# Performance work log

Measured on AMD Instinct MI355X. Metric: run time of the kernel, lower is better.

## Reference

```python
import jax, jax.numpy as jnp
import numpy as np

N = 20000          # nodes
E = 320000         # edges (avg degree 16)
G = 256            # graphs in batch
NUM_TACTICS = 1000
NUM_TYPES = 3
TYPE_D = 32
TAC_D = 64
H = 512
IN_D = TYPE_D + TAC_D  # 96


def setup_inputs() -> dict:
    key = jax.random.key(0)
    ks = jax.random.split(key, 16)
    node_type = jax.random.randint(ks[0], (N,), 0, NUM_TYPES)
    # tactic id in {-1, 0..num_tactics-1}
    node_tactic_id = jax.random.randint(ks[1], (N,), 0, NUM_TACTICS + 1) - 1
    edge_index = jax.random.randint(ks[2], (2, E), 0, N)
    batch = jnp.sort(jax.random.randint(ks[3], (N,), 0, G))
    s = 0.02
    p = {
        'type_emb': jax.random.normal(ks[4], (NUM_TYPES, TYPE_D), jnp.float32) * s,
        'tactic_emb': jax.random.normal(ks[5], (NUM_TACTICS + 1, TAC_D), jnp.float32) * s,
        'W1l': jax.random.normal(ks[6], (H, IN_D), jnp.float32) * s,
        'b1l': jnp.zeros((H,), jnp.float32),
        'W1r': jax.random.normal(ks[7], (H, IN_D), jnp.float32) * s,
        'W2l': jax.random.normal(ks[8], (H, H), jnp.float32) * s,
        'b2l': jnp.zeros((H,), jnp.float32),
        'W2r': jax.random.normal(ks[9], (H, H), jnp.float32) * s,
        'Wc1': jax.random.normal(ks[10], (H, H), jnp.float32) * s,
        'bc1': jnp.zeros((H,), jnp.float32),
        'Wc2': jax.random.normal(ks[11], (NUM_TACTICS, H), jnp.float32) * s,
        'bc2': jnp.zeros((NUM_TACTICS,), jnp.float32),
    }
    return dict(node_type=node_type, node_tactic_id=node_tactic_id,
                edge_index=edge_index, batch=batch, **p)


def _sage_conv(x, src, dst, Wl, bl, Wr):
    # PyG SAGEConv (aggr='mean'): out = lin_l(mean_{j in N(i)} x_j) + lin_r(x_i)
    msg = x[src]                                              # [E, D]
    ssum = jax.ops.segment_sum(msg, dst, num_segments=N)      # [N, D]
    cnt = jax.ops.segment_sum(jnp.ones((src.shape[0],), x.dtype), dst,
                              num_segments=N)                 # [N]
    agg = ssum / jnp.maximum(cnt, 1.0)[:, None]
    return agg @ Wl.T + bl + x @ Wr.T


def reference(node_type, node_tactic_id, edge_index, batch,
              type_emb, tactic_emb, W1l, b1l, W1r, W2l, b2l, W2r,
              Wc1, bc1, Wc2, bc2):
    t_type = type_emb[node_type]                              # [N, 32]
    shifted = jnp.clip(node_tactic_id + 1, 0, NUM_TACTICS)
    t_tac = tactic_emb[shifted]                               # [N, 64]
    x = jnp.concatenate([t_type, t_tac], axis=-1)             # [N, 96]

    src, dst = edge_index[0], edge_index[1]
    x = jax.nn.relu(_sage_conv(x, src, dst, W1l, b1l, W1r))   # [N, H]
    x = _sage_conv(x, src, dst, W2l, b2l, W2r)                # [N, H]

    # global mean pool over graphs
    gsum = jax.ops.segment_sum(x, batch, num_segments=G)      # [G, H]
    gcnt = jax.ops.segment_sum(jnp.ones((N,), x.dtype), batch, num_segments=G)
    graph_repr = gsum / jnp.maximum(gcnt, 1.0)[:, None]

    h = jax.nn.relu(graph_repr @ Wc1.T + bc1)
    logits = h @ Wc2.T + bc2                                  # [G, num_tactics]
    return logits
```

## Files before the change

kernel.cpp:

```cpp
#include <hip/hip_runtime.h>

#define N_NODES 20000
#define N_EDGES 320000
#define NGRAPH  256
#define NTAC    1000
#define HD      512
#define NC      25
#define KCH     800

typedef __attribute__((ext_vector_type(8))) short bf16x8;
typedef __attribute__((ext_vector_type(4))) short short4v;
typedef __attribute__((ext_vector_type(4))) float f32x4;

__device__ __forceinline__ short f2bf(float f) {
  union { float f; unsigned u; } v; v.f = f;
  unsigned r = v.u + 0x7FFFu + ((v.u >> 16) & 1u);
  return (short)(r >> 16);
}
__device__ __forceinline__ float bf2f(short s) {
  union { unsigned u; float f; } v;
  v.u = ((unsigned)(unsigned short)s) << 16;
  return v.f;
}
__device__ __forceinline__ bf16x8 cast8(const float* p) {
  float4 v0 = *reinterpret_cast<const float4*>(p);
  float4 v1 = *reinterpret_cast<const float4*>(p + 4);
  bf16x8 o;
  o[0] = f2bf(v0.x); o[1] = f2bf(v0.y); o[2] = f2bf(v0.z); o[3] = f2bf(v0.w);
  o[4] = f2bf(v1.x); o[5] = f2bf(v1.y); o[6] = f2bf(v1.z); o[7] = f2bf(v1.w);
  return o;
}
__device__ __forceinline__ void gload16(const void* g, void* l) {
  __builtin_amdgcn_global_load_lds((const __attribute__((address_space(1))) void*)g,
                                   (__attribute__((address_space(3))) void*)l,
                                   16, 0, 0);
}

__global__ void k_front(const float* __restrict__ Wc1, const float* __restrict__ Wc2,
                        short* __restrict__ WC1B, short* __restrict__ WC2B,
                        const float* __restrict__ W1l, const float* __restrict__ W1r,
                        short* __restrict__ BC1,
                        const float* __restrict__ W2l, const float* __restrict__ W2r,
                        short* __restrict__ BC2,
                        const int* __restrict__ ntype, const int* __restrict__ ntac,
                        const float* __restrict__ temb, const float* __restrict__ tacemb,
                        short* __restrict__ A1,
                        const int* __restrict__ dst, int* __restrict__ deg,
                        const int* __restrict__ batch, int* __restrict__ rstart,
                        float* __restrict__ COEF, short* __restrict__ COEFB) {
  int idx = blockIdx.x * 256 + threadIdx.x;
  const int S0 = HD * HD / 8;
  const int S1 = NTAC * HD / 8;
  const int S2 = HD * 192 / 8;
  const int S3 = HD * 1024 / 8;
  const int S4 = N_NODES * 24;
  const int S5 = N_EDGES;
  const int S6 = N_NODES;
  const int S7 = NGRAPH * N_NODES / 4;
  const int S8 = NGRAPH * N_NODES / 8;
  if (idx < S0) {
    *reinterpret_cast<bf16x8*>(&WC1B[idx * 8]) = cast8(&Wc1[idx * 8]);
  } else if ((idx -= S0) < S1) {
    *reinterpret_cast<bf16x8*>(&WC2B[idx * 8]) = cast8(&Wc2[idx * 8]);
  } else if ((idx -= S1) < S2) {
    int n = idx / 24, k8 = idx - n * 24;
    const float* s = (k8 < 12) ? &W1l[(size_t)n * 96 + k8 * 8]
                               : &W1r[(size_t)n * 96 + (k8 - 12) * 8];
    *reinterpret_cast<bf16x8*>(&BC1[(size_t)n * 192 + k8 * 8]) = cast8(s);
  } else if ((idx -= S2) < S3) {
    int n = idx >> 7, k8 = idx & 127;
    const float* s = (k8 < 64) ? &W2l[(size_t)n * 512 + k8 * 8]
                               : &W2r[(size_t)n * 512 + (k8 - 64) * 8];
    *reinterpret_cast<bf16x8*>(&BC2[(size_t)n * 1024 + k8 * 8]) = cast8(s);
  } else if ((idx -= S3) < S4) {
    int node = idx / 24;
    int j = idx - node * 24;
    float4 v;
    int col;
    if (j < 8) {
      int t = ntype[node];
      v = *reinterpret_cast<const float4*>(&temb[t * 32 + j * 4]);
      col = j * 4;
    } else {
      int s = ntac[node] + 1;
      s = s < 0 ? 0 : (s > NTAC ? NTAC : s);
      v = *reinterpret_cast<const float4*>(&tacemb[s * 64 + (j - 8) * 4]);
      col = 32 + (j - 8) * 4;
    }
    short4v o = {f2bf(v.x), f2bf(v.y), f2bf(v.z), f2bf(v.w)};
    *reinterpret_cast<short4v*>(&A1[(size_t)node * 192 + 96 + col]) = o;
  } else if ((idx -= S4) < S5) {
    atomicAdd(&deg[dst[idx]], 1);
  } else if ((idx -= S5) < S6) {
    int i = idx;
    int b = batch[i];
    int bp = (i == 0) ? -1 : batch[i - 1];
    for (int g = bp + 1; g <= b; ++g) rstart[g] = i;
    if (i == N_NODES - 1)
      for (int g = b + 1; g <= NGRAPH; ++g) rstart[g] = N_NODES;
  } else if ((idx -= S6) < S7) {
    float4 z = {0.f, 0.f, 0.f, 0.f};
    *reinterpret_cast<float4*>(&COEF[(size_t)idx * 4]) = z;
  } else if ((idx -= S7) < S8) {
    bf16x8 z = {0, 0, 0, 0, 0, 0, 0, 0};
    *reinterpret_cast<bf16x8*>(&COEFB[(size_t)NGRAPH * N_NODES + (size_t)idx * 8]) = z;
  }
}

__global__ __launch_bounds__(1024) void k_scan(const int* __restrict__ deg,
                                               int* __restrict__ rowstart) {
  __shared__ int partial[1024];
  const int t = threadIdx.x;
  const int CH = (N_NODES + 1023) / 1024;
  int s = 0;
  for (int i = 0; i < CH; ++i) {
    int idx = t * CH + i;
    if (idx < N_NODES) s += deg[idx];
  }
  partial[t] = s;
  __syncthreads();
  for (int off = 1; off < 1024; off <<= 1) {
    int v = (t >= off) ? partial[t - off] : 0;
    __syncthreads();
    partial[t] += v;
    __syncthreads();
  }
  int run = (t == 0) ? 0 : partial[t - 1];
  for (int i = 0; i < CH; ++i) {
    int idx = t * CH + i;
    if (idx < N_NODES) { rowstart[idx] = run; run += deg[idx]; }
  }
  if (t == 1023) rowstart[N_NODES] = run;
}

__global__ void k_scatter(const int* __restrict__ src, const int* __restrict__ dst,
                          const int* __restrict__ rows, int* __restrict__ deg,
                          int* __restrict__ esrc, const int* __restrict__ batch,
                          const int* __restrict__ rstart,
                          float* __restrict__ COEF, short* __restrict__ COEFB) {
  int idx = blockIdx.x * 256 + threadIdx.x;
  if (idx < N_EDGES) {
    int d = dst[idx];
    int old = atomicSub(&deg[d], 1);
    int p = rows[d + 1] - old;
    int sj = src[idx];
    esrc[p] = sj;
    int g = batch[d];
    float invd = 1.0f / (float)max(rows[d + 1] - rows[d], 1);
    float invg = 1.0f / (float)max(rstart[g + 1] - rstart[g], 1);
    atomicAdd(&COEF[(size_t)g * N_NODES + sj], invd * invg);
  } else if ((idx -= N_EDGES) < N_NODES) {
    int j = idx;
    int g = batch[j];
    float invg = 1.0f / (float)max(rstart[g + 1] - rstart[g], 1);
    COEFB[(size_t)(NGRAPH + g) * N_NODES + j] = f2bf(invg);
  }
}

__global__ __launch_bounds__(256) void k_mid(
    const float* __restrict__ COEF, short* __restrict__ COEFB,
    const int* __restrict__ rowstart, const int* __restrict__ esrc,
    short* __restrict__ A1) {
  int idx = blockIdx.x * 256 + threadIdx.x;
  const int SC = NGRAPH * N_NODES / 8;
  if (idx < SC) {
    int r = idx / 2500, k8 = (idx - r * 2500) * 8;
    *reinterpret_cast<bf16x8*>(&COEFB[(size_t)r * N_NODES + k8]) =
        cast8(&COEF[(size_t)r * N_NODES + k8]);
    return;
  }
  idx -= SC;
  if (idx >= N_NODES * 24) return;
  int node = idx / 24;
  int c = (idx - node * 24) * 4;
  const int s0 = rowstart[node], s1 = rowstart[node + 1];
  float a0 = 0.f, a1 = 0.f, a2 = 0.f, a3 = 0.f;
  for (int i = s0; i < s1; ++i) {
    int nbr = esrc[i];
    short4v v = *reinterpret_cast<const short4v*>(&A1[(size_t)nbr * 192 + 96 + c]);
    a0 += bf2f(v[0]); a1 += bf2f(v[1]); a2 += bf2f(v[2]); a3 += bf2f(v[3]);
  }
  const float inv = 1.0f / fmaxf((float)(s1 - s0), 1.0f);
  short4v o = {f2bf(a0 * inv), f2bf(a1 * inv), f2bf(a2 * inv), f2bf(a3 * inv)};
  *reinterpret_cast<short4v*>(&A1[(size_t)node * 192 + c]) = o;
}

__global__ __launch_bounds__(256) void k_gemm_l1(
    const short* __restrict__ A, const short* __restrict__ B,
    const float* __restrict__ bias, short* __restrict__ X1T, int nxp) {
  constexpr int K = 192;
  __shared__ short smem[32768];
  const int lin = blockIdx.x;
  const int pnl = (lin & 7) + ((lin >> 5) << 3);
  const int cbk = (lin >> 3) & 3;
  if (pnl >= nxp) return;
  const int m0 = pnl * 128, n0 = cbk * 128;
  const int t = threadIdx.x;
  const int l = t & 63, wid = t >> 6;
  const int wr = (wid >> 1) * 64, wc = (wid & 1) * 64;
  const int fr = l & 15, fs = l >> 4;

  f32x4 acc[4][4];
#pragma unroll
  for (int a = 0; a < 4; ++a)
#pragma unroll
    for (int b = 0; b < 4; ++b) acc[a][b] = (f32x4){0.f, 0.f, 0.f, 0.f};

  const int idx0 = t, r0 = idx0 >> 2, sp0 = idx0 & 3;
  const int sl0 = (sp0 - (r0 >> 1)) & 3;
  const int idx1 = t + 256, r1 = idx1 >> 2, sp1 = idx1 & 3;
  const int sl1 = (sp1 - (r1 >> 1)) & 3;
  int rowA0 = m0 + r0; rowA0 = rowA0 < N_NODES ? rowA0 : N_NODES - 1;
  int rowA1 = m0 + r1; rowA1 = rowA1 < N_NODES ? rowA1 : N_NODES - 1;
  const short* Ap0 = A + (size_t)rowA0 * K + sl0 * 8;
  const short* Ap1 = A + (size_t)rowA1 * K + sl1 * 8;
  const short* Bp0 = B + (size_t)(n0 + r0) * K + sl0 * 8;
  const short* Bp1 = B + (size_t)(n0 + r1) * K + sl1 * 8;
  constexpr int NK = K / 32;

#define STAGE1(bo, k0)                                 \
  gload16(Ap0 + (k0), &smem[(bo) + idx0 * 8]);         \
  gload16(Bp0 + (k0), &smem[(bo) + 4096 + idx0 * 8]);  \
  gload16(Ap1 + (k0), &smem[(bo) + idx1 * 8]);         \
  gload16(Bp1 + (k0), &smem[(bo) + 4096 + idx1 * 8]);

#define COMPUTE1(bo) {                                                             \
  bf16x8 av[4], bv[4];                                                             \
  _Pragma("unroll")                                                                \
  for (int mi = 0; mi < 4; ++mi) {                                                 \
    const int r = wr + mi * 16 + fr;                                               \
    av[mi] = *reinterpret_cast<const bf16x8*>(                                     \
        &smem[(bo) + r * 32 + ((fs + (r >> 1)) & 3) * 8]);                         \
  }                                                                                \
  _Pragma("unroll")                                                                \
  for (int ni = 0; ni < 4; ++ni) {                                                 \
    const int r = wc + ni * 16 + fr;                                               \
    bv[ni] = *reinterpret_cast<const bf16x8*>(                                     \
        &smem[(bo) + 4096 + r * 32 + ((fs + (r >> 1)) & 3) * 8]);                  \
  }                                                                                \
  _Pragma("unroll")                                                                \
  for (int mi = 0; mi < 4; ++mi)                                                   \
    _Pragma("unroll")                                                              \
    for (int ni = 0; ni < 4; ++ni)                                                 \
      acc[mi][ni] = __builtin_amdgcn_mfma_f32_16x16x32_bf16(av[mi], bv[ni],        \
                                                            acc[mi][ni], 0, 0, 0); }

  STAGE1(0, 0)
  STAGE1(8192, 32)
  STAGE1(16384, 64)
#pragma unroll
  for (int k = 0; k < NK; ++k) {
    if (k + 2 <= NK - 1)      { asm volatile("s_waitcnt vmcnt(8)" ::: "memory"); }
    else if (k + 1 <= NK - 1) { asm volatile("s_waitcnt vmcnt(4)" ::: "memory"); }
    else                      { asm volatile("s_waitcnt vmcnt(0)" ::: "memory"); }
    __builtin_amdgcn_s_barrier();
    if (k + 3 < NK) { STAGE1(((k + 3) & 3) * 8192, (k + 3) * 32) }
    COMPUTE1((k & 3) * 8192)
  }
#undef STAGE1
#undef COMPUTE1

  __syncthreads();
#pragma unroll
  for (int ni = 0; ni < 4; ++ni) {
    const int colL = wc + ni * 16 + fr;
    const float bb = bias[n0 + colL];
#pragma unroll
    for (int mi = 0; mi < 4; ++mi) {
      const f32x4 c = acc[mi][ni];
#pragma unroll
      for (int i = 0; i < 4; ++i) {
        const int rowL = wr + mi * 16 + fs * 4 + i;
        smem[colL * 136 + rowL] = f2bf(fmaxf(c[i] + bb, 0.f));
      }
    }
  }
  __syncthreads();
#pragma unroll
  for (int q = 0; q < 8; ++q) {
    const int it = q * 256 + t;
    const int cr = it >> 4, n8 = (it & 15) << 3;
    if (m0 + n8 < N_NODES)
      *reinterpret_cast<bf16x8*>(&X1T[(size_t)(n0 + cr) * N_NODES + m0 + n8]) =
          *reinterpret_cast<const bf16x8*>(&smem[cr * 136 + n8]);
  }
}

__global__ __launch_bounds__(256) void k_bigemm(
    const short* __restrict__ A,
    const short* __restrict__ B,
    float* __restrict__ CP) {
  __shared__ short smem[32768];
  const int x = blockIdx.x & 7;
  const int slot = blockIdx.x >> 3;
  const int chunk = x + 8 * (slot >> 4);
  if (chunk >= NC) return;
  const int sub = slot & 15;
  const int panel = sub >> 2, sib = sub & 3;
  const int m0 = panel * 128, n0 = sib * 128;
  const int kb = chunk * KCH;
  const int t = threadIdx.x;
  const int l = t & 63, wid = t >> 6;
  const int wr = (wid >> 1) * 64, wc = (wid & 1) * 64;
  const int fr = l & 15, fs = l >> 4;

  f32x4 acc[4][4];
#pragma unroll
  for (int a = 0; a < 4; ++a)
#pragma unroll
    for (int b = 0; b < 4; ++b) acc[a][b] = (f32x4){0.f, 0.f, 0.f, 0.f};

  const int idx0 = t, r0 = idx0 >> 2, sp0 = idx0 & 3;
  const int sl0 = (sp0 - (r0 >> 1)) & 3;
  const int idx1 = t + 256, r1 = idx1 >> 2, sp1 = idx1 & 3;
  const int sl1 = (sp1 - (r1 >> 1)) & 3;
  const short* Ap0 = A + (size_t)(m0 + r0) * N_NODES + kb + sl0 * 8;
  const short* Ap1 = A + (size_t)(m0 + r1) * N_NODES + kb + sl1 * 8;
  const short* Bp0 = B + (size_t)(n0 + r0) * N_NODES + kb + sl0 * 8;
  const short* Bp1 = B + (size_t)(n0 + r1) * N_NODES + kb + sl1 * 8;
  constexpr int NK = KCH / 32;

#define STAGE2(bo, k0)                                 \
  gload16(Ap0 + (k0), &smem[(bo) + idx0 * 8]);         \
  gload16(Bp0 + (k0), &smem[(bo) + 4096 + idx0 * 8]);  \
  gload16(Ap1 + (k0), &smem[(bo) + idx1 * 8]);         \
  gload16(Bp1 + (k0), &smem[(bo) + 4096 + idx1 * 8]);

#define COMPUTE2(bo) {                                                             \
  bf16x8 av[4], bv[4];                                                             \
  _Pragma("unroll")                                                                \
  for (int mi = 0; mi < 4; ++mi) {                                                 \
    const int r = wr + mi * 16 + fr;                                               \
    av[mi] = *reinterpret_cast<const bf16x8*>(                                     \
        &smem[(bo) + r * 32 + ((fs + (r >> 1)) & 3) * 8]);                         \
  }                                                                                \
  _Pragma("unroll")                                                                \
  for (int ni = 0; ni < 4; ++ni) {                                                 \
    const int r = wc + ni * 16 + fr;                                               \
    bv[ni] = *reinterpret_cast<const bf16x8*>(                                     \
        &smem[(bo) + 4096 + r * 32 + ((fs + (r >> 1)) & 3) * 8]);                  \
  }                                                                                \
  _Pragma("unroll")                                                                \
  for (int mi = 0; mi < 4; ++mi)                                                   \
    _Pragma("unroll")                                                              \
    for (int ni = 0; ni < 4; ++ni)                                                 \
      acc[mi][ni] = __builtin_amdgcn_mfma_f32_16x16x32_bf16(av[mi], bv[ni],        \
                                                            acc[mi][ni], 0, 0, 0); }

  STAGE2(0, 0)
  STAGE2(8192, 32)
  STAGE2(16384, 64)
  for (int k = 0; k < NK; ++k) {
    if (k + 2 <= NK - 1)      { asm volatile("s_waitcnt vmcnt(8)" ::: "memory"); }
    else if (k + 1 <= NK - 1) { asm volatile("s_waitcnt vmcnt(4)" ::: "memory"); }
    else                      { asm volatile("s_waitcnt vmcnt(0)" ::: "memory"); }
    __builtin_amdgcn_s_barrier();
    if (k + 3 < NK) { STAGE2(((k + 3) & 3) * 8192, (k + 3) * 32) }
    COMPUTE2((k & 3) * 8192)
  }
#undef STAGE2
#undef COMPUTE2

  __syncthreads();
  float* smemf = reinterpret_cast<float*>(smem);
  for (int half = 0; half < 2; ++half) {
    if (wr == half * 64) {
#pragma unroll
      for (int ni = 0; ni < 4; ++ni) {
        const int colL = wc + ni * 16 + fr;
#pragma unroll
        for (int mi = 0; mi < 4; ++mi) {
          const f32x4 c = acc[mi][ni];
#pragma unroll
          for (int i = 0; i < 4; ++i) {
            const int row = mi * 16 + fs * 4 + i;
            smemf[row * 132 + colL] = c[i];
          }
        }
      }
    }
    __syncthreads();
#pragma unroll
    for (int q = 0; q < 8; ++q) {
      const int it = q * 256 + t;
      const int row = it >> 5, c4 = (it & 31) * 4;
      *reinterpret_cast<f32x4*>(
          &CP[((size_t)chunk * 512 + m0 + half * 64 + row) * 512 + n0 + c4]) =
          *reinterpret_cast<const f32x4*>(&smemf[row * 132 + c4]);
    }
    __syncthreads();
  }
}

__global__ __launch_bounds__(256) void k_redP(const float* __restrict__ CP,
                                              short* __restrict__ PB) {
  int it = blockIdx.x * 256 + threadIdx.x;
  int r = it >> 7, c4 = (it & 127) * 4;
  f32x4 s = (f32x4){0.f, 0.f, 0.f, 0.f};
  for (int ch = 0; ch < NC; ++ch) {
    f32x4 v = *reinterpret_cast<const f32x4*>(&CP[((size_t)ch * 512 + r) * 512 + c4]);
    s[0] += v[0]; s[1] += v[1]; s[2] += v[2]; s[3] += v[3];
  }
  int g = r & 255, off = (r >> 8) * 512;
  short4v o = {f2bf(s[0]), f2bf(s[1]), f2bf(s[2]), f2bf(s[3])};
  *reinterpret_cast<short4v*>(&PB[(size_t)g * 1024 + off + c4]) = o;
}

template<int K, bool RELU, bool F32OUT>
__device__ __forceinline__ void cls_gemm(
    const short* __restrict__ A, const short* __restrict__ B,
    const float* __restrict__ bias,
    short* __restrict__ outS, int ostride, float* __restrict__ outF) {
  __shared__ short smem[32768];
  const int bx = blockIdx.x;
  const int m0 = (bx & 1) * 128;
  const int n0 = (bx >> 1) * 128;
  const int t = threadIdx.x;
  const int l = t & 63, wid = t >> 6;
  const int wr = (wid >> 1) * 64, wc = (wid & 1) * 64;
  const int fr = l & 15, fs = l >> 4;

  f32x4 acc[4][4];
#pragma unroll
  for (int a = 0; a < 4; ++a)
#pragma unroll
    for (int b = 0; b < 4; ++b) acc[a][b] = (f32x4){0.f, 0.f, 0.f, 0.f};

  const int idx0 = t, r0 = idx0 >> 2, sp0 = idx0 & 3;
  const int sl0 = (sp0 - (r0 >> 1)) & 3;
  const int idx1 = t + 256, r1 = idx1 >> 2, sp1 = idx1 & 3;
  const int sl1 = (sp1 - (r1 >> 1)) & 3;
  const short* Ap0 = A + (size_t)(m0 + r0) * K + sl0 * 8;
  const short* Ap1 = A + (size_t)(m0 + r1) * K + sl1 * 8;
  const short* Bp0 = B + (size_t)(n0 + r0) * K + sl0 * 8;
  const short* Bp1 = B + (size_t)(n0 + r1) * K + sl1 * 8;
  constexpr int NK = K / 32;

#define STAGE3(bo, k0)                                 \
  gload16(Ap0 + (k0), &smem[(bo) + idx0 * 8]);         \
  gload16(Bp0 + (k0), &smem[(bo) + 4096 + idx0 * 8]);  \
  gload16(Ap1 + (k0), &smem[(bo) + idx1 * 8]);         \
  gload16(Bp1 + (k0), &smem[(bo) + 4096 + idx1 * 8]);

#define COMPUTE3(bo) {                                                             \
  bf16x8 av[4], bv[4];                                                             \
  _Pragma("unroll")                                                                \
  for (int mi = 0; mi < 4; ++mi) {                                                 \
    const int r = wr + mi * 16 + fr;                                               \
    av[mi] = *reinterpret_cast<const bf16x8*>(                                     \
        &smem[(bo) + r * 32 + ((fs + (r >> 1)) & 3) * 8]);                         \
  }                                                                                \
  _Pragma("unroll")                                                                \
  for (int ni = 0; ni < 4; ++ni) {                                                 \
    const int r = wc + ni * 16 + fr;                                               \
    bv[ni] = *reinterpret_cast<const bf16x8*>(                                     \
        &smem[(bo) + 4096 + r * 32 + ((fs + (r >> 1)) & 3) * 8]);                  \
  }                                                                                \
  _Pragma("unroll")                                                                \
  for (int mi = 0; mi < 4; ++mi)                                                   \
    _Pragma("unroll")                                                              \
    for (int ni = 0; ni < 4; ++ni)                                                 \
      acc[mi][ni] = __builtin_amdgcn_mfma_f32_16x16x32_bf16(av[mi], bv[ni],        \
                                                            acc[mi][ni], 0, 0, 0); }

  STAGE3(0, 0)
  STAGE3(8192, 32)
  STAGE3(16384, 64)
  for (int k = 0; k < NK; ++k) {
    if (k + 2 <= NK - 1)      { asm volatile("s_waitcnt vmcnt(8)" ::: "memory"); }
    else if (k + 1 <= NK - 1) { asm volatile("s_waitcnt vmcnt(4)" ::: "memory"); }
    else                      { asm volatile("s_waitcnt vmcnt(0)" ::: "memory"); }
    __builtin_amdgcn_s_barrier();
    if (k + 3 < NK) { STAGE3(((k + 3) & 3) * 8192, (k + 3) * 32) }
    COMPUTE3((k & 3) * 8192)
  }
#undef STAGE3
#undef COMPUTE3

  __syncthreads();
  if constexpr (!F32OUT) {
#pragma unroll
    for (int ni = 0; ni < 4; ++ni) {
      const int colL = wc + ni * 16 + fr;
      const float bb = bias[n0 + colL];
#pragma unroll
      for (int mi = 0; mi < 4; ++mi) {
        const f32x4 c = acc[mi][ni];
#pragma unroll
        for (int i = 0; i < 4; ++i) {
          const int rowL = wr + mi * 16 + fs * 4 + i;
          float v = c[i] + bb;
          if (RELU) v = fmaxf(v, 0.f);
          smem[rowL * 136 + colL] = f2bf(v);
        }
      }
    }
    __syncthreads();
#pragma unroll
    for (int pz = 0; pz < 8; ++pz) {
      const int idx = pz * 256 + t;
      const int row = idx >> 4, c8 = (idx & 15) << 3;
      *reinterpret_cast<bf16x8*>(&outS[(size_t)(m0 + row) * ostride + n0 + c8]) =
          *reinterpret_cast<const bf16x8*>(&smem[row * 136 + c8]);
    }
  } else {
    float* smemf = reinterpret_cast<float*>(smem);
    for (int half = 0; half < 2; ++half) {
      if (wr == half * 64) {
#pragma unroll
        for (int ni = 0; ni < 4; ++ni) {
          const int colL = wc + ni * 16 + fr;
          const float bb = bias[n0 + colL];
#pragma unroll
          for (int mi = 0; mi < 4; ++mi) {
            const f32x4 c = acc[mi][ni];
#pragma unroll
            for (int i = 0; i < 4; ++i) {
              const int row = mi * 16 + fs * 4 + i;
              smemf[row * 132 + colL] = c[i] + bb;
            }
          }
        }
      }
      __syncthreads();
#pragma unroll
      for (int q = 0; q < 8; ++q) {
        const int it = q * 256 + t;
        const int row = it >> 5, c4 = (it & 31) * 4;
        if (n0 + c4 < NTAC)
          *reinterpret_cast<f32x4*>(
              &outF[(size_t)(m0 + half * 64 + row) * NTAC + n0 + c4]) =
              *reinterpret_cast<const f32x4*>(&smemf[row * 132 + c4]);
      }
      __syncthreads();
    }
  }
}

__global__ __launch_bounds__(256) void k_cls1(
    const short* __restrict__ A, const short* __restrict__ B,
    const float* __restrict__ bias, short* __restrict__ outS) {
  cls_gemm<1024, false, false>(A, B, bias, outS, 512, nullptr);
}
__global__ __launch_bounds__(256) void k_cls2(
    const short* __restrict__ A, const short* __restrict__ B,
    const float* __restrict__ bias, short* __restrict__ outS) {
  cls_gemm<512, true, false>(A, B, bias, outS, 512, nullptr);
}
__global__ __launch_bounds__(256) void k_cls3(
    const short* __restrict__ A, const short* __restrict__ B,
    const float* __restrict__ bias, float* __restrict__ outF) {
  cls_gemm<512, false, true>(A, B, bias, nullptr, 0, outF);
}

extern "C" void kernel_launch(void* const* d_in, const int* in_sizes, int n_in,
                              void* d_out, int out_size, void* d_ws, size_t ws_size,
                              hipStream_t stream) {
  const int*   node_type = (const int*)d_in[0];
  const int*   node_tac  = (const int*)d_in[1];
  const int*   edge      = (const int*)d_in[2];
  const int*   batch     = (const int*)d_in[3];
  const float* temb      = (const float*)d_in[4];
  const float* tacemb    = (const float*)d_in[5];
  const float* W1l       = (const float*)d_in[6];
  const float* b1l       = (const float*)d_in[7];
  const float* W1r       = (const float*)d_in[8];
  const float* W2l       = (const float*)d_in[9];
  const float* b2l       = (const float*)d_in[10];
  const float* W2r       = (const float*)d_in[11];
  const float* Wc1       = (const float*)d_in[12];
  const float* bc1       = (const float*)d_in[13];
  const float* Wc2       = (const float*)d_in[14];
  const float* bc2       = (const float*)d_in[15];
  const int* src = edge;
  const int* dst = edge + N_EDGES;

  char* p = (char*)d_ws;
  int*   DEG    = (int*)p;    p += N_NODES * 4;
  int*   ROWS   = (int*)p;    p += (N_NODES + 4) * 4;
  int*   RSTART = (int*)p;    p += (NGRAPH + 4) * 4;
  int*   ESRC   = (int*)p;    p += N_EDGES * 4;
  short* A1     = (short*)p;  p += (size_t)N_NODES * 192 * 2;
  short* X1T    = (short*)p;  p += (size_t)HD * N_NODES * 2;
  float* COEF   = (float*)p;  p += (size_t)NGRAPH * N_NODES * 4;
  short* COEFB  = (short*)p;  p += (size_t)2 * NGRAPH * N_NODES * 2;
  float* CP     = (float*)p;  p += (size_t)NC * 512 * 512 * 4;
  short* PB     = (short*)p;  p += NGRAPH * 1024 * 2;
  short* GRB    = (short*)p;  p += NGRAPH * HD * 2;
  short* HSB    = (short*)p;  p += NGRAPH * HD * 2;
  short* BC1    = (short*)p;  p += HD * 192 * 2;
  short* BC2    = (short*)p;  p += HD * 1024 * 2;
  short* WC1B   = (short*)p;  p += HD * HD * 2;
  short* WC2B   = (short*)p;  p += (size_t)1024 * HD * 2;

  hipMemsetAsync(DEG, 0, N_NODES * 4, stream);

  const int front_items = HD * HD / 8 + NTAC * HD / 8 + HD * 192 / 8 +
                          HD * 1024 / 8 + N_NODES * 24 + N_EDGES + N_NODES +
                          NGRAPH * N_NODES / 4 + NGRAPH * N_NODES / 8;
  k_front<<<(front_items + 255) / 256, 256, 0, stream>>>(
      Wc1, Wc2, WC1B, WC2B, W1l, W1r, BC1, W2l, W2r, BC2,
      node_type, node_tac, temb, tacemb, A1, dst, DEG, batch, RSTART, COEF, COEFB);

  k_scan<<<1, 1024, 0, stream>>>(DEG, ROWS);
  k_scatter<<<(N_EDGES + N_NODES + 255) / 256, 256, 0, stream>>>(
      src, dst, ROWS, DEG, ESRC, batch, RSTART, COEF, COEFB);

  const int mid_items = NGRAPH * N_NODES / 8 + N_NODES * 24;
  k_mid<<<(mid_items + 255) / 256, 256, 0, stream>>>(COEF, COEFB, ROWS, ESRC, A1);

  const int NXP = (N_NODES + 127) / 128;
  k_gemm_l1<<<640, 256, 0, stream>>>(A1, BC1, b1l, X1T, NXP);

  k_bigemm<<<512, 256, 0, stream>>>(COEFB, X1T, CP);
  k_redP<<<256, 256, 0, stream>>>(CP, PB);
  k_cls1<<<8, 256, 0, stream>>>(PB, BC2, b2l, GRB);
  k_cls2<<<8, 256, 0, stream>>>(GRB, WC1B, bc1, HSB);
  k_cls3<<<16, 256, 0, stream>>>(HSB, WC2B, bc2, (float*)d_out);
}
```

Baseline: 199.5 us.

## Fuse graph mean-pool of layer-1 output into GEMM epilogue, halve bigemm rows

The per-graph mean of X1 (the lin_r term of layer 2) was computed as a second block of 256 rows in the big coefficient GEMM using a dense invg matrix. It is now accumulated in the layer-1 GEMM epilogue as segmented per-graph run sums with float atomics into PX, exploiting sorted batch ids. The pooled sum is scaled by 1/graph size in k_redP. This halves the bigemm work, the COEFB and CP buffers and the zero-fill, at the cost of an extra serial 64-step loop and atomics in the layer-1 GEMM epilogue.

Result: no change. 202.7 us (+1.6%).

```diff
diff --git a/kernel.cpp b/kernel.cpp
--- a/kernel.cpp
+++ b/kernel.cpp
@@ -47,7 +47,7 @@
                         short* __restrict__ A1,
                         const int* __restrict__ dst, int* __restrict__ deg,
                         const int* __restrict__ batch, int* __restrict__ rstart,
-                        float* __restrict__ COEF, short* __restrict__ COEFB) {
+                        float* __restrict__ COEF, float* __restrict__ PX) {
   int idx = blockIdx.x * 256 + threadIdx.x;
   const int S0 = HD * HD / 8;
   const int S1 = NTAC * HD / 8;
@@ -57,7 +57,7 @@
   const int S5 = N_EDGES;
   const int S6 = N_NODES;
   const int S7 = NGRAPH * N_NODES / 4;
-  const int S8 = NGRAPH * N_NODES / 8;
+  const int S8 = NGRAPH * HD / 4;
   if (idx < S0) {
     *reinterpret_cast<bf16x8*>(&WC1B[idx * 8]) = cast8(&Wc1[idx * 8]);
   } else if ((idx -= S0) < S1) {
@@ -102,8 +102,8 @@
     float4 z = {0.f, 0.f, 0.f, 0.f};
     *reinterpret_cast<float4*>(&COEF[(size_t)idx * 4]) = z;
   } else if ((idx -= S7) < S8) {
-    bf16x8 z = {0, 0, 0, 0, 0, 0, 0, 0};
-    *reinterpret_cast<bf16x8*>(&COEFB[(size_t)NGRAPH * N_NODES + (size_t)idx * 8]) = z;
+    float4 z = {0.f, 0.f, 0.f, 0.f};
+    *reinterpret_cast<float4*>(&PX[(size_t)idx * 4]) = z;
   }
 }
 
@@ -137,24 +137,18 @@
                           const int* __restrict__ rows, int* __restrict__ deg,
                           int* __restrict__ esrc, const int* __restrict__ batch,
                           const int* __restrict__ rstart,
-                          float* __restrict__ COEF, short* __restrict__ COEFB) {
+                          float* __restrict__ COEF) {
   int idx = blockIdx.x * 256 + threadIdx.x;
-  if (idx < N_EDGES) {
-    int d = dst[idx];
-    int old = atomicSub(&deg[d], 1);
-    int p = rows[d + 1] - old;
-    int sj = src[idx];
-    esrc[p] = sj;
-    int g = batch[d];
-    float invd = 1.0f / (float)max(rows[d + 1] - rows[d], 1);
-    float invg = 1.0f / (float)max(rstart[g + 1] - rstart[g], 1);
-    atomicAdd(&COEF[(size_t)g * N_NODES + sj], invd * invg);
-  } else if ((idx -= N_EDGES) < N_NODES) {
-    int j = idx;
-    int g = batch[j];
-    float invg = 1.0f / (float)max(rstart[g + 1] - rstart[g], 1);
-    COEFB[(size_t)(NGRAPH + g) * N_NODES + j] = f2bf(invg);
-  }
+  if (idx >= N_EDGES) return;
+  int d = dst[idx];
+  int old = atomicSub(&deg[d], 1);
+  int p = rows[d + 1] - old;
+  int sj = src[idx];
+  esrc[p] = sj;
+  int g = batch[d];
+  float invd = 1.0f / (float)max(rows[d + 1] - rows[d], 1);
+  float invg = 1.0f / (float)max(rstart[g + 1] - rstart[g], 1);
+  atomicAdd(&COEF[(size_t)g * N_NODES + sj], invd * invg);
 }
 
 __global__ __launch_bounds__(256) void k_mid(
@@ -187,9 +181,11 @@
 
 __global__ __launch_bounds__(256) void k_gemm_l1(
     const short* __restrict__ A, const short* __restrict__ B,
-    const float* __restrict__ bias, short* __restrict__ X1T, int nxp) {
+    const float* __restrict__ bias, const int* __restrict__ batch,
+    short* __restrict__ X1T, float* __restrict__ PX, int nxp) {
   constexpr int K = 192;
   __shared__ short smem[32768];
+  __shared__ int bsh[128];
   const int lin = blockIdx.x;
   const int pnl = (lin & 7) + ((lin >> 5) << 3);
   const int cbk = (lin >> 3) & 3;
@@ -261,6 +257,10 @@
 #undef COMPUTE1
 
   __syncthreads();
+  if (t < 128) {
+    int node = m0 + t;
+    bsh[t] = batch[node < N_NODES ? node : N_NODES - 1];
+  }
 #pragma unroll
   for (int ni = 0; ni < 4; ++ni) {
     const int colL = wc + ni * 16 + fr;
@@ -283,6 +283,24 @@
     if (m0 + n8 < N_NODES)
       *reinterpret_cast<bf16x8*>(&X1T[(size_t)(n0 + cr) * N_NODES + m0 + n8]) =
           *reinterpret_cast<const bf16x8*>(&smem[cr * 136 + n8]);
+  }
+  {
+    const int colp = t >> 1, hf = t & 1;
+    float run = 0.f;
+    int curg = -1;
+    for (int i = 0; i < 64; ++i) {
+      const int node = m0 + hf * 64 + i;
+      if (node >= N_NODES) break;
+      const int g = bsh[hf * 64 + i];
+      const float v = bf2f(smem[colp * 136 + hf * 64 + i]);
+      if (g != curg) {
+        if (curg >= 0) atomicAdd(&PX[(size_t)curg * HD + n0 + colp], run);
+        curg = g; run = v;
+      } else {
+        run += v;
+      }
+    }
+    if (curg >= 0) atomicAdd(&PX[(size_t)curg * HD + n0 + colp], run);
   }
 }
 
@@ -293,9 +311,9 @@
   __shared__ short smem[32768];
   const int x = blockIdx.x & 7;
   const int slot = blockIdx.x >> 3;
-  const int chunk = x + 8 * (slot >> 4);
+  const int chunk = x + 8 * (slot >> 3);
   if (chunk >= NC) return;
-  const int sub = slot & 15;
+  const int sub = slot & 7;
   const int panel = sub >> 2, sib = sub & 3;
   const int m0 = panel * 128, n0 = sib * 128;
   const int kb = chunk * KCH;
@@ -385,7 +403,7 @@
       const int it = q * 256 + t;
       const int row = it >> 5, c4 = (it & 31) * 4;
       *reinterpret_cast<f32x4*>(
-          &CP[((size_t)chunk * 512 + m0 + half * 64 + row) * 512 + n0 + c4]) =
+          &CP[((size_t)chunk * 256 + m0 + half * 64 + row) * 512 + n0 + c4]) =
           *reinterpret_cast<const f32x4*>(&smemf[row * 132 + c4]);
     }
     __syncthreads();
@@ -393,17 +411,29 @@
 }
 
 __global__ __launch_bounds__(256) void k_redP(const float* __restrict__ CP,
+                                              const float* __restrict__ PX,
+                                              const int* __restrict__ rstart,
                                               short* __restrict__ PB) {
   int it = blockIdx.x * 256 + threadIdx.x;
-  int r = it >> 7, c4 = (it & 127) * 4;
-  f32x4 s = (f32x4){0.f, 0.f, 0.f, 0.f};
-  for (int ch = 0; ch < NC; ++ch) {
-    f32x4 v = *reinterpret_cast<const f32x4*>(&CP[((size_t)ch * 512 + r) * 512 + c4]);
-    s[0] += v[0]; s[1] += v[1]; s[2] += v[2]; s[3] += v[3];
-  }
-  int g = r & 255, off = (r >> 8) * 512;
-  short4v o = {f2bf(s[0]), f2bf(s[1]), f2bf(s[2]), f2bf(s[3])};
-  *reinterpret_cast<short4v*>(&PB[(size_t)g * 1024 + off + c4]) = o;
+  if (it < 32768) {
+    int g = it >> 7, c4 = (it & 127) * 4;
+    f32x4 s = (f32x4){0.f, 0.f, 0.f, 0.f};
+    for (int ch = 0; ch < NC; ++ch) {
+      f32x4 v = *reinterpret_cast<const f32x4*>(
+          &CP[((size_t)ch * 256 + g) * 512 + c4]);
+      s[0] += v[0]; s[1] += v[1]; s[2] += v[2]; s[3] += v[3];
+    }
+    short4v o = {f2bf(s[0]), f2bf(s[1]), f2bf(s[2]), f2bf(s[3])};
+    *reinterpret_cast<short4v*>(&PB[(size_t)g * 1024 + c4]) = o;
+  } else {
+    it -= 32768;
+    int g = it >> 7, c4 = (it & 127) * 4;
+    const float invg = 1.0f / fmaxf((float)(rstart[g + 1] - rstart[g]), 1.0f);
+    f32x4 v = *reinterpret_cast<const f32x4*>(&PX[(size_t)g * HD + c4]);
+    short4v o = {f2bf(v[0] * invg), f2bf(v[1] * invg),
+                 f2bf(v[2] * invg), f2bf(v[3] * invg)};
+    *reinterpret_cast<short4v*>(&PB[(size_t)g * 1024 + 512 + c4]) = o;
+  }
 }
 
 template<int K, bool RELU, bool F32OUT>
@@ -583,8 +613,9 @@
   short* A1     = (short*)p;  p += (size_t)N_NODES * 192 * 2;
   short* X1T    = (short*)p;  p += (size_t)HD * N_NODES * 2;
   float* COEF   = (float*)p;  p += (size_t)NGRAPH * N_NODES * 4;
-  short* COEFB  = (short*)p;  p += (size_t)2 * NGRAPH * N_NODES * 2;
-  float* CP     = (float*)p;  p += (size_t)NC * 512 * 512 * 4;
+  short* COEFB  = (short*)p;  p += (size_t)NGRAPH * N_NODES * 2;
+  float* PX     = (float*)p;  p += NGRAPH * HD * 4;
+  float* CP     = (float*)p;  p += (size_t)NC * 256 * 512 * 4;
   short* PB     = (short*)p;  p += NGRAPH * 1024 * 2;
   short* GRB    = (short*)p;  p += NGRAPH * HD * 2;
   short* HSB    = (short*)p;  p += NGRAPH * HD * 2;
@@ -597,23 +628,23 @@
 
   const int front_items = HD * HD / 8 + NTAC * HD / 8 + HD * 192 / 8 +
                           HD * 1024 / 8 + N_NODES * 24 + N_EDGES + N_NODES +
-                          NGRAPH * N_NODES / 4 + NGRAPH * N_NODES / 8;
+                          NGRAPH * N_NODES / 4 + NGRAPH * HD / 4;
   k_front<<<(front_items + 255) / 256, 256, 0, stream>>>(
       Wc1, Wc2, WC1B, WC2B, W1l, W1r, BC1, W2l, W2r, BC2,
-      node_type, node_tac, temb, tacemb, A1, dst, DEG, batch, RSTART, COEF, COEFB);
+      node_type, node_tac, temb, tacemb, A1, dst, DEG, batch, RSTART, COEF, PX);
 
   k_scan<<<1, 1024, 0, stream>>>(DEG, ROWS);
-  k_scatter<<<(N_EDGES + N_NODES + 255) / 256, 256, 0, stream>>>(
-      src, dst, ROWS, DEG, ESRC, batch, RSTART, COEF, COEFB);
+  k_scatter<<<(N_EDGES + 255) / 256, 256, 0, stream>>>(
+      src, dst, ROWS, DEG, ESRC, batch, RSTART, COEF);
 
   const int mid_items = NGRAPH * N_NODES / 8 + N_NODES * 24;
   k_mid<<<(mid_items + 255) / 256, 256, 0, stream>>>(COEF, COEFB, ROWS, ESRC, A1);
 
   const int NXP = (N_NODES + 127) / 128;
-  k_gemm_l1<<<640, 256, 0, stream>>>(A1, BC1, b1l, X1T, NXP);
-
-  k_bigemm<<<512, 256, 0, stream>>>(COEFB, X1T, CP);
-  k_redP<<<256, 256, 0, stream>>>(CP, PB);
+  k_gemm_l1<<<640, 256, 0, stream>>>(A1, BC1, b1l, batch, X1T, PX, NXP);
+
+  k_bigemm<<<256, 256, 0, stream>>>(COEFB, X1T, CP);
+  k_redP<<<256, 256, 0, stream>>>(CP, PX, RSTART, PB);
   k_cls1<<<8, 256, 0, stream>>>(PB, BC2, b2l, GRB);
   k_cls2<<<8, 256, 0, stream>>>(GRB, WC1B, bc1, HSB);
   k_cls3<<<16, 256, 0, stream>>>(HSB, WC2B, bc2, (float*)d_out);
```
